# Optimization experiments

Measured on AMD Instinct MI355X. Metric: run time of the kernel, lower is better.

## Reference

```python
import jax, jax.numpy as jnp
import numpy as np
from jax.scipy.special import gammaln

# sizes (see shape_source)
N_CELLS = 1024
N_GENES = 1000
N_LATENT = 50
NB_ENC = 16          # encoder histogram bins per gene
NB_DEC = 16          # decoder mixture components (sum(n_decoder_bins))
N_HID = 16           # encoder hidden dim
N_CUTS = 4_000_000
N_FRAGS = 2_000_000
N_TOTAL_CELLS = 10_000
N_TOTAL_CUTS = 50_000_000
BN_EPS = 1e-5


def _normal_logprob(x, loc, scale):
    z = (x - loc) / scale
    return -0.5 * z * z - jnp.log(scale) - 0.5 * jnp.log(2.0 * jnp.pi)


def setup_inputs() -> dict:
    key = jax.random.key(0)
    ks = jax.random.split(key, 20)
    cut_coordinates = jax.random.uniform(ks[0], (N_CUTS,), dtype=jnp.float32)
    cut_cell = jax.random.randint(ks[1], (N_CUTS,), 0, N_CELLS)
    cut_local_gene_ix = jax.random.randint(ks[2], (N_CUTS,), 0, N_GENES)
    cut_local_cellxgene_ix = cut_cell * N_GENES + cut_local_gene_ix
    local_cellxgene_ix = jax.random.randint(ks[3], (N_FRAGS,), 0, N_CELLS * N_GENES)
    genes_oi = jnp.arange(N_GENES)
    cells_oi = jnp.arange(N_CELLS)
    eps = jax.random.normal(ks[4], (N_CELLS, N_LATENT), dtype=jnp.float32)
    n_in = N_GENES * NB_ENC
    enc_W1 = jax.random.normal(ks[5], (n_in, N_HID)) * (1.0 / np.sqrt(n_in))
    enc_b1 = jnp.zeros((N_HID,))
    bn_gamma = jnp.ones((N_HID,))
    bn_beta = jnp.zeros((N_HID,))
    W_loc = jax.random.normal(ks[6], (N_HID, N_LATENT)) * (1.0 / np.sqrt(N_HID))
    b_loc = jnp.zeros((N_LATENT,))
    W_scale = jax.random.normal(ks[7], (N_HID, N_LATENT)) * (1.0 / np.sqrt(N_HID))
    b_scale = jnp.zeros((N_LATENT,))
    logit_weight = jax.random.normal(ks[8], (N_GENES, N_LATENT, NB_DEC)) * 0.05
    rho_weight = jax.random.normal(ks[9], (N_GENES, N_LATENT)) * 0.05
    baseline_heights = jax.random.normal(ks[10], (N_GENES, NB_DEC)) * 0.1
    libsize = jax.random.randint(ks[11], (N_TOTAL_CELLS,), 1000, 20000)
    rho_bias = jax.random.uniform(ks[12], (N_GENES,), minval=1e-4, maxval=1e-2)
    return dict(
        cut_coordinates=cut_coordinates, eps=eps,
        enc_W1=enc_W1, enc_b1=enc_b1, bn_gamma=bn_gamma, bn_beta=bn_beta,
        W_loc=W_loc, b_loc=b_loc, W_scale=W_scale, b_scale=b_scale,
        logit_weight=logit_weight, rho_weight=rho_weight,
        baseline_heights=baseline_heights, rho_bias=rho_bias,
        cut_local_cellxgene_ix=cut_local_cellxgene_ix,
        cut_local_gene_ix=cut_local_gene_ix,
        local_cellxgene_ix=local_cellxgene_ix,
        genes_oi=genes_oi, cells_oi=cells_oi, libsize=libsize,
    )


def reference(cut_coordinates, eps, enc_W1, enc_b1, bn_gamma, bn_beta,
              W_loc, b_loc, W_scale, b_scale, logit_weight, rho_weight,
              baseline_heights, rho_bias, cut_local_cellxgene_ix,
              cut_local_gene_ix, local_cellxgene_ix, genes_oi, cells_oi,
              libsize):
    n_cells = cells_oi.shape[0]
    n_genes = genes_oi.shape[0]

    # ---- Encoder: digitize + bincount histogram ----
    bin_enc = jnp.minimum(jnp.floor(cut_coordinates * NB_ENC), NB_ENC - 1).astype(jnp.int32)
    digitized = bin_enc + cut_local_cellxgene_ix.astype(jnp.int32) * NB_ENC
    counts = jax.ops.segment_sum(jnp.ones_like(cut_coordinates), digitized,
                                 num_segments=n_cells * n_genes * NB_ENC)
    x = jnp.log1p(counts.reshape(n_cells, n_genes * NB_ENC))  # [C, G*NB]

    h = x @ enc_W1 + enc_b1
    mu = h.mean(axis=0)
    var = h.var(axis=0)  # biased, matches torch BN in train mode
    h = (h - mu) / jnp.sqrt(var + BN_EPS) * bn_gamma + bn_beta
    h = jax.nn.relu(h)
    loc = h @ W_loc + b_loc                 # [C, L]
    scale = jnp.exp(h @ W_scale + b_scale)  # [C, L]

    # ---- latent sample + KL ----
    q_scale = scale * 0.1
    latent = loc + q_scale * eps
    latent_kl = (_normal_logprob(latent, 0.0, 1.0)
                 - _normal_logprob(latent, loc, q_scale)) * (N_TOTAL_CELLS / n_cells)

    # ---- Decoder (n_layers=0: per-gene linear heads) ----
    lw = logit_weight[genes_oi]                       # [G, L, K]
    rw = rho_weight[genes_oi]                         # [G, L]
    mixture_delta = jnp.einsum('cl,glk->cgk', latent, lw)  # [C, G, K]
    rho_delta = jnp.einsum('cl,gl->cg', latent, rw)        # [C, G]
    md_cxg = mixture_delta.reshape(n_cells * n_genes, NB_DEC)
    md_cut = md_cxg[cut_local_cellxgene_ix]           # [N_CUTS, K] gather
    mixture_delta_kl = _normal_logprob(lw, 0.0, 0.1)

    # ---- mixture likelihood: piecewise-constant spline density per cut ----
    logits = baseline_heights[cut_local_gene_ix] + md_cut  # [N_CUTS, K]
    logp = jax.nn.log_softmax(logits, axis=-1)
    bin_dec = jnp.minimum(jnp.floor(cut_coordinates * NB_DEC), NB_DEC - 1).astype(jnp.int32)
    likelihood_mixture = (jnp.take_along_axis(logp, bin_dec[:, None], axis=1)[:, 0]
                          + jnp.log(float(NB_DEC)))

    # ---- fragment-count Poisson likelihood ----
    fragexpr = (rho_bias[genes_oi][None, :] * jnp.exp(rho_delta)
                * libsize[cells_oi].astype(jnp.float32)[:, None])  # [C, G]
    fragmentcounts = jax.ops.segment_sum(
        jnp.ones((local_cellxgene_ix.shape[0],), jnp.float32),
        local_cellxgene_ix, num_segments=n_cells * n_genes
    ).reshape(n_cells, n_genes)
    likelihood_frag = (fragmentcounts * jnp.log(fragexpr) - fragexpr
                       - gammaln(fragmentcounts + 1.0))

    rho_delta_kl = _normal_logprob(rw, 0.0, 0.1)

    likelihood = (likelihood_mixture.sum() * (N_TOTAL_CUTS / cut_coordinates.shape[0])
                  + likelihood_frag.sum() * (N_TOTAL_CELLS / n_cells))
    elbo = (-likelihood - latent_kl.sum() - mixture_delta_kl.sum()
            - rho_delta_kl.sum())
    return elbo
```

## Files before the change

### kernel.cpp

```cpp
#include <hip/hip_runtime.h>
#include <hip/hip_bf16.h>
#include <math.h>


#define G_      1000
#define C_      1024
#define L_      50
#define K_      16
#define NHID_   16
#define CUT_SCALE   12.5f
#define CELL_SCALE  9.765625f

#define CHUNK_    6144
#define RCAP_CUT  18432
#define RCAP_FRAG 9216

#define GCNTC_OFF  0ull
#define GCNTF_OFF  1024ull
#define DONE_OFF   2048ull
#define DACC_OFF   6400ull
#define HT_OFF     6912ull
#define ZERO_BYTES 72448ull
#define LATBF_OFF  72448ull
#define LWT_OFF    203520ull
#define ENTC_OFF   2251520ull
#define ENTF_OFF   11688704ull
#define MERGED_OFF 16407296ull
#define FRAGU8_OFF 24599296ull
#define LATT_OFF   25623296ull
#define WS_NEED    25828096ull

typedef __attribute__((ext_vector_type(8))) short short8;
typedef __attribute__((ext_vector_type(4))) float f32x4;

__device__ __constant__ float LGT[32] = {
    0.0f, 0.0f, 0.6931471805599453f, 1.791759469228055f, 3.1780538303479458f,
    4.787491742782046f, 6.579251212010101f, 8.525161361065415f,
    10.60460290274525f, 12.801827480081469f, 15.104412573075516f,
    17.502307845873887f, 19.987214495661885f, 22.552163853123425f,
    25.19122118273868f, 27.89927138384089f, 30.671860106080672f,
    33.50507345013689f, 36.39544520803305f, 39.339884187199495f,
    42.335616460753485f, 45.38013889847691f, 48.47118135183523f,
    51.60667556776438f, 54.78472939811232f, 58.00360522298052f,
    61.261701761002f, 64.55753862700633f, 67.88974313718154f,
    71.25703896716801f, 74.65823634883016f, 78.0922235533153f };

__device__ __forceinline__ double atomAddF64(double* p, double v) {
    return __hip_atomic_fetch_add(p, v, __ATOMIC_RELAXED,
                                  __HIP_MEMORY_SCOPE_AGENT);
}

__device__ __forceinline__ float block_sum_256(float v) {
    __shared__ float sm[256];
    int t = threadIdx.x;
    __syncthreads();
    sm[t] = v;
    __syncthreads();
#pragma unroll
    for (int s = 128; s > 0; s >>= 1) {
        if (t < s) sm[t] += sm[t + s];
        __syncthreads();
    }
    return sm[0];
}

__global__ __launch_bounds__(256)
void part_kernel(const int* __restrict__ cut_ix,
                 const float* __restrict__ coord,
                 const int* __restrict__ frag_ix,
                 unsigned int* __restrict__ gcnt_c,
                 unsigned int* __restrict__ gcnt_f,
                 unsigned short* __restrict__ entc,
                 unsigned short* __restrict__ entf,
                 const float* __restrict__ lw,
                 const float* __restrict__ rw,
                 __hip_bfloat16* __restrict__ lwT,
                 double* __restrict__ dacc,
                 int n_cuts, int n_frags, int ncc, int nblk_part) {
    int t = threadIdx.x;
    int bid = blockIdx.x;
    if (bid >= nblk_part) {
        int r = bid - nblk_part;
        if (r < 256) {
            for (int g = r; g < G_; g += 256) {
                for (int i = t; i < L_ * K_; i += 256) {
                    float v = lw[(size_t)g * (L_ * K_) + i];
                    lwT[(size_t)g * 1024 + (i & 15) * 64 + (i >> 4)] =
                        __float2bfloat16(v);
                }
                for (int i = t; i < 16 * 14; i += 256) {
                    int n = i / 14, l = 50 + (i % 14);
                    lwT[(size_t)g * 1024 + n * 64 + l] = __float2bfloat16(0.f);
                }
            }
        } else {
            const int NTOT = G_ * L_ * K_ + G_ * L_;
            int wb = r - 256;
            float s = 0.f;
            for (int i = wb * 256 + t; i < NTOT; i += 256 * 256) {
                float w = (i < G_ * L_ * K_) ? lw[i] : rw[i - G_ * L_ * K_];
                s += fmaf(-50.f * w, w, 1.3836465597893733f);
            }
            s = block_sum_256(s);
            if (t == 0) atomAddF64(&dacc[wb & 63], (double)(-s));
        }
        return;
    }
    __shared__ unsigned int cnt[256], excl[256], cur[256], gbas[256];
    __shared__ unsigned short stage[CHUNK_];
    __shared__ unsigned char bkof[CHUNK_];
    bool isCut = (bid < ncc);
    int blk = isCut ? bid : bid - ncc;
    const int* idx = isCut ? cut_ix : frag_ix;
    int n = isCut ? n_cuts : n_frags;
    int rcap = isCut ? RCAP_CUT : RCAP_FRAG;
    unsigned int* gcount = isCut ? gcnt_c : gcnt_f;
    unsigned short* ent = isCut ? entc : entf;
    int i0 = blk * CHUNK_;
    cnt[t] = 0;
    int4 I[6]; float4 X[6];
    unsigned int vm;
    bool full = (i0 + CHUNK_ <= n);
    if (full) {
        const int4* ip = (const int4*)(idx + i0);
#pragma unroll
        for (int k = 0; k < 6; ++k) I[k] = ip[k * 256 + t];
        if (isCut) {
            const float4* xp = (const float4*)(coord + i0);
#pragma unroll
            for (int k = 0; k < 6; ++k) X[k] = xp[k * 256 + t];
        }
        vm = 0xFFFFFFu;
    } else {
        vm = 0;
#pragma unroll
        for (int k = 0; k < 6; ++k) {
            int r0 = i0 + (k * 256 + t) * 4;
            int* Ii = (int*)&I[k]; float* Xi = (float*)&X[k];
#pragma unroll
            for (int u = 0; u < 4; ++u) {
                bool v = (r0 + u) < n;
                if (v) vm |= 1u << (k * 4 + u);
                Ii[u] = v ? idx[r0 + u] : 0;
                Xi[u] = (v && isCut) ? coord[r0 + u] : 0.f;
            }
        }
    }
    __syncthreads();
#pragma unroll
    for (int k = 0; k < 6; ++k) {
        const int* Ii = (const int*)&I[k];
        const float* Xi = (const float*)&X[k];
#pragma unroll
        for (int u = 0; u < 4; ++u) {
            if (vm & (1u << (k * 4 + u))) {
                int ix = Ii[u];
                int c = ix / G_;
                int g = ix - c * G_;
                unsigned int bk;
                if (isCut) {
                    int b = (int)(Xi[u] * 16.f); b = b > 15 ? 15 : b;
                    bk = ((unsigned)(c >> 6) << 4) | ((unsigned)(g * K_ + b) >> 10);
                } else {
                    bk = ((unsigned)(c >> 6) << 4) | ((unsigned)g >> 6);
                }
                atomicAdd(&cnt[bk], 1u);
            }
        }
    }
    __syncthreads();
    if (t < 64) {
        unsigned int c0 = cnt[t * 4 + 0], c1 = cnt[t * 4 + 1];
        unsigned int c2 = cnt[t * 4 + 2], c3 = cnt[t * 4 + 3];
        unsigned int tot = c0 + c1 + c2 + c3;
        unsigned int run = tot;
#pragma unroll
        for (int o = 1; o < 64; o <<= 1) {
            unsigned int v = __shfl_up(run, o, 64);
            if (t >= o) run += v;
        }
        unsigned int base = run - tot;
        excl[t * 4 + 0] = base;
        excl[t * 4 + 1] = base + c0;
        excl[t * 4 + 2] = base + c0 + c1;
        excl[t * 4 + 3] = base + c0 + c1 + c2;
    }
    __syncthreads();
    gbas[t] = cnt[t] ? atomicAdd(&gcount[t], cnt[t]) : 0u;
    cur[t] = excl[t];
    __syncthreads();
#pragma unroll
    for (int k = 0; k < 6; ++k) {
        const int* Ii = (const int*)&I[k];
        const float* Xi = (const float*)&X[k];
#pragma unroll
        for (int u = 0; u < 4; ++u) {
            if (vm & (1u << (k * 4 + u))) {
                int ix = Ii[u];
                int c = ix / G_;
                int g = ix - c * G_;
                unsigned int bk; unsigned short e;
                if (isCut) {
                    int b = (int)(Xi[u] * 16.f); b = b > 15 ? 15 : b;
                    int bin = g * K_ + b;
                    bk = ((unsigned)(c >> 6) << 4) | ((unsigned)bin >> 10);
                    e = (unsigned short)(((c & 63) << 10) | (bin & 1023));
                } else {
                    bk = ((unsigned)(c >> 6) << 4) | ((unsigned)g >> 6);
                    e = (unsigned short)(((c & 63) << 6) | (g & 63));
                }
                unsigned int p = atomicAdd(&cur[bk], 1u);
                stage[p] = e;
                bkof[p] = (unsigned char)bk;
            }
        }
    }
    __syncthreads();
    int total = n - i0; if (total > CHUNK_) total = CHUNK_;
    for (int p = t; p < total; p += 256) {
        unsigned int bk = bkof[p];
        unsigned int dst = gbas[bk] + (p - excl[bk]);
        if (dst < (unsigned)rcap)
            ent[(size_t)bk * rcap + dst] = stage[p];
    }
}

__global__ __launch_bounds__(256)
void mid_kernel(const unsigned int* __restrict__ gcnt_c,
                const unsigned short* __restrict__ entc,
                const unsigned int* __restrict__ gcnt_f,
                const unsigned short* __restrict__ entf,
                const float* __restrict__ W1,
                unsigned int* __restrict__ merged,
                unsigned int* __restrict__ fragw,
                float* __restrict__ hT) {
    __shared__ unsigned int h[8192];
    __shared__ float w1s[4096];
    int t = threadIdx.x;
    int bid = blockIdx.x;
    if (bid < 256) {
        int bk = bid;
        int cg = bk >> 4, bc = bk & 15;
        for (int i = t; i < 8192; i += 256) h[i] = 0;
        __syncthreads();
        unsigned int count = gcnt_c[bk];
        if (count > RCAP_CUT) count = RCAP_CUT;
        const unsigned int* e32 = (const unsigned int*)(entc + (size_t)bk * RCAP_CUT);
        unsigned int npair = count >> 1;
        for (unsigned int base = 0; base < npair; base += 1024) {
            unsigned int w[4]; bool val[4];
#pragma unroll
            for (int u = 0; u < 4; ++u) {
                unsigned int p = base + u * 256 + t;
                val[u] = (p < npair);
                w[u] = val[u] ? e32[p] : 0u;
            }
#pragma unroll
            for (int u = 0; u < 4; ++u) {
                if (val[u]) {
                    unsigned int v0 = w[u] & 0xffffu, v1 = w[u] >> 16;
                    unsigned int c0 = v0 >> 10, c1 = v1 >> 10;
                    atomicAdd(&h[(v0 & 1023u) * 8 + (c0 >> 3)],
                              1u << ((c0 & 7) * 4));
                    atomicAdd(&h[(v1 & 1023u) * 8 + (c1 >> 3)],
                              1u << ((c1 & 7) * 4));
                }
            }
        }
        if (t == 0 && (count & 1u)) {
            unsigned int v = ((const unsigned short*)e32)[count - 1];
            unsigned int c0 = v >> 10;
            atomicAdd(&h[(v & 1023u) * 8 + (c0 >> 3)], 1u << ((c0 & 7) * 4));
        }
        __syncthreads();
        for (int i = t; i < 8192; i += 256) {
            int bin = bc * 1024 + (i >> 3);
            if (bin < 16000)
                merged[(unsigned)bin * 128u + (unsigned)cg * 8u + (i & 7)] = h[i];
        }
        int c_lo = t & 63, sub = t >> 6;
        float acc[NHID_];
#pragma unroll
        for (int j = 0; j < NHID_; ++j) acc[j] = 0.f;
        int sh = (c_lo & 7) * 4;
        for (int qq = 0; qq < 4; ++qq) {
            __syncthreads();
            int wbase = (bc * 1024 + qq * 256) * NHID_;
#pragma unroll
            for (int r = 0; r < 16; ++r) {
                int i = r * 256 + t;
                int gi = wbase + i;
                w1s[i] = (gi < 16000 * NHID_) ? W1[gi] : 0.f;
            }
            __syncthreads();
            const float4* w1v = (const float4*)w1s;
            int rl0 = qq * 256 + sub * 64;
#pragma unroll 2
            for (int bl = 0; bl < 64; ++bl) {
                int row = bc * 1024 + rl0 + bl;
                if (row < 16000) {
                    int rh = rl0 + bl;
                    int rw2 = sub * 64 + bl;
                    unsigned int w = h[rh * 8 + (c_lo >> 3)];
                    float xv = __logf((float)(((w >> sh) & 0xfu) + 1u));
                    float4 wa = w1v[rw2 * 4 + 0];
                    float4 wb = w1v[rw2 * 4 + 1];
                    float4 wc = w1v[rw2 * 4 + 2];
                    float4 wd = w1v[rw2 * 4 + 3];
                    acc[0] = fmaf(xv, wa.x, acc[0]);  acc[1] = fmaf(xv, wa.y, acc[1]);
                    acc[2] = fmaf(xv, wa.z, acc[2]);  acc[3] = fmaf(xv, wa.w, acc[3]);
                    acc[4] = fmaf(xv, wb.x, acc[4]);  acc[5] = fmaf(xv, wb.y, acc[5]);
                    acc[6] = fmaf(xv, wb.z, acc[6]);  acc[7] = fmaf(xv, wb.w, acc[7]);
                    acc[8] = fmaf(xv, wc.x, acc[8]);  acc[9] = fmaf(xv, wc.y, acc[9]);
                    acc[10] = fmaf(xv, wc.z, acc[10]); acc[11] = fmaf(xv, wc.w, acc[11]);
                    acc[12] = fmaf(xv, wd.x, acc[12]); acc[13] = fmaf(xv, wd.y, acc[13]);
                    acc[14] = fmaf(xv, wd.z, acc[14]); acc[15] = fmaf(xv, wd.w, acc[15]);
                }
            }
        }
        __syncthreads();
        float* sp = (float*)w1s;
#pragma unroll
        for (int j = 0; j < NHID_; ++j) sp[sub * 1024 + j * 64 + c_lo] = acc[j];
        __syncthreads();
        for (int i = t; i < 1024; i += 256) {
            int j = i >> 6, c = i & 63;
            float v = sp[j * 64 + c] + sp[1024 + j * 64 + c]
                    + sp[2048 + j * 64 + c] + sp[3072 + j * 64 + c];
            atomicAdd(&hT[j * C_ + cg * 64 + c], v);
        }
    } else {
        int bk = bid - 256, cg = bk >> 4, gc = bk & 15;
        for (int i = t; i < 2048; i += 256) h[i] = 0;
        __syncthreads();
        unsigned int count = gcnt_f[bk];
        if (count > RCAP_FRAG) count = RCAP_FRAG;
        const unsigned short* e = entf + (size_t)bk * RCAP_FRAG;
#pragma unroll 4
        for (unsigned int p = t; p < count; p += 256) {
            unsigned int v = e[p];
            unsigned int g_lo = v & 63u;
            unsigned int c_lo = (v >> 6) & 63u;
            atomicAdd(&h[g_lo * 32 + (c_lo >> 1)], 1u << ((c_lo & 1) * 16));
        }
        __syncthreads();
        for (int i = t; i < 1024; i += 256) {
            int g_lo = i >> 4, wb = i & 15;
            unsigned int lo = h[g_lo * 32 + wb * 2];
            unsigned int hi = h[g_lo * 32 + wb * 2 + 1];
            unsigned int outv = (lo & 0xffu) | (((lo >> 16) & 0xffu) << 8)
                              | ((hi & 0xffu) << 16) | (((hi >> 16) & 0xffu) << 24);
            int g = gc * 64 + g_lo;
            if (g < G_)
                fragw[(unsigned)g * 256u + (unsigned)cg * 16u + wb] = outv;
        }
    }
}

__global__ __launch_bounds__(256)
void latent_kernel(const float* __restrict__ hT,
                   const float* __restrict__ gamma,
                   const float* __restrict__ beta,
                   const float* __restrict__ W_loc,
                   const float* __restrict__ b_loc,
                   const float* __restrict__ W_scale,
                   const float* __restrict__ b_scale,
                   const float* __restrict__ eps,
                   float* __restrict__ latT,
                   __hip_bfloat16* __restrict__ latbf,
                   double* __restrict__ dacc) {
    __shared__ float scs[NHID_], shs[NHID_];
    int t = threadIdx.x;
    {
        int j = t >> 4, cl = t & 15;
        double s1 = 0.0, s2 = 0.0;
#pragma unroll 8
        for (int k = 0; k < 64; ++k) {
            float v = hT[j * C_ + cl + k * 16];
            s1 += (double)v; s2 += (double)v * (double)v;
        }
#pragma unroll
        for (int m = 1; m < 16; m <<= 1) {
            s1 += __shfl_xor(s1, m);
            s2 += __shfl_xor(s2, m);
        }
        if (cl == 0) {
            double mean = s1 * (1.0 / C_);
            double var = s2 * (1.0 / C_) - mean * mean;
            float rstd = rsqrtf((float)var + 1e-5f);
            float sc = gamma[j] * rstd;
            scs[j] = sc;
            shs[j] = beta[j] - (float)mean * sc;
        }
    }
    __syncthreads();
    int idx = blockIdx.x * 256 + t;
    float kl = 0.f;
    {
        int c = idx / L_;
        int l = idx - c * L_;
        float hb[NHID_];
#pragma unroll
        for (int j = 0; j < NHID_; ++j) {
            float v = fmaf(hT[j * C_ + c], scs[j], shs[j]);
            hb[j] = v > 0.f ? v : 0.f;
        }
        float loc = b_loc[l], ls = b_scale[l];
#pragma unroll
        for (int j = 0; j < NHID_; ++j) {
            loc = fmaf(hb[j], W_loc[j * L_ + l], loc);
            ls  = fmaf(hb[j], W_scale[j * L_ + l], ls);
        }
        float qs = 0.1f * __expf(ls);
        float e = eps[idx];
        float lat = fmaf(qs, e, loc);
        latT[(size_t)l * C_ + c] = lat;
        latbf[c * 64 + l] = __float2bfloat16(lat);
        if (l < 14) latbf[c * 64 + 50 + l] = __float2bfloat16(0.f);
        float z = (lat - loc) / qs;
        kl = fmaf(-0.5f * lat, lat, fmaf(0.5f * z, z, __logf(qs)));
    }
    float s = block_sum_256(kl);
    if (threadIdx.x == 0)
        atomAddF64(&dacc[blockIdx.x & 63], (double)(-CELL_SCALE * s));
}

__global__ __launch_bounds__(256)
void mixpois_kernel(const __hip_bfloat16* __restrict__ latbf,
                    const __hip_bfloat16* __restrict__ lwT,
                    const unsigned int* __restrict__ merged,
                    const float* __restrict__ baseline,
                    const float* __restrict__ latT,
                    const float* __restrict__ rw,
                    const float* __restrict__ rho_bias,
                    const int* __restrict__ libsize,
                    const unsigned char* __restrict__ fragb,
                    double* __restrict__ dacc,
                    unsigned int* __restrict__ done,
                    float* __restrict__ out) {
    int g = blockIdx.x;
    int y = blockIdx.y;
    int t = threadIdx.x;
    int lane = t & 63;
    int wv = t >> 6;
    int s16 = lane & 15;
    int quad = lane >> 4;
    const __hip_bfloat16* bb = lwT + (size_t)g * 1024 + s16 * 64 + quad * 8;
    short8 lw1 = *(const short8*)bb;
    short8 lw2 = *(const short8*)(bb + 32);
    const float4 bl4 = *(const float4*)(baseline + g * K_ + quad * 4);
    const unsigned int* mrow =
        merged + (size_t)(g * K_ + quad * 4) * 128u;
    float partial = 0.f;
    int cwave = y * 256 + wv * 64;
#pragma unroll
    for (int mt = 0; mt < 4; ++mt) {
        int c0 = cwave + mt * 16;
        const __hip_bfloat16* aa = latbf + (size_t)(c0 + s16) * 64 + quad * 8;
        short8 la1 = *(const short8*)aa;
        short8 la2 = *(const short8*)(aa + 32);
        f32x4 d = {bl4.x, bl4.y, bl4.z, bl4.w};
        d = __builtin_amdgcn_mfma_f32_16x16x32_bf16(lw1, la1, d, 0, 0, 0);
        d = __builtin_amdgcn_mfma_f32_16x16x32_bf16(lw2, la2, d, 0, 0, 0);
        float m = fmaxf(fmaxf(d[0], d[1]), fmaxf(d[2], d[3]));
        m = fmaxf(m, __shfl_xor(m, 16));
        m = fmaxf(m, __shfl_xor(m, 32));
        float e0 = __expf(d[0] - m), e1 = __expf(d[1] - m);
        float e2 = __expf(d[2] - m), e3 = __expf(d[3] - m);
        float S = (e0 + e1) + (e2 + e3);
        S += __shfl_xor(S, 16);
        S += __shfl_xor(S, 32);
        float lse = m + __logf(S);
        int cp = c0 + s16;
        unsigned int widx = (unsigned)cp >> 3;
        int sb = (cp & 7) * 4;
#pragma unroll
        for (int r = 0; r < 4; ++r) {
            float cnt = (float)((mrow[r * 128u + widx] >> sb) & 0xfu);
            partial = fmaf(cnt, d[r] - lse, partial);
        }
    }
    float v;
    {
        int c = y * 256 + t;
        const float* rwg = rw + (size_t)g * L_;
        float rho = 0.f;
#pragma unroll 10
        for (int l = 0; l < L_; ++l)
            rho = fmaf(latT[l * C_ + c], rwg[l], rho);
        unsigned int fc = fragb[(size_t)g * C_ + c];
        float fe = rho_bias[g] * __expf(rho) * (float)libsize[c];
        float lf = fmaf((float)fc, __logf(fe), -fe) - LGT[fc > 31u ? 31u : fc];
        v = fmaf(-CUT_SCALE, partial, -CELL_SCALE * lf);
    }
    float contrib = block_sum_256(v);
    __shared__ int lastflag;
    if (threadIdx.x == 0) {
        lastflag = 0;
        int slot = blockIdx.x & 63;
        double oldv = atomAddF64(&dacc[slot], (double)contrib);
        unsigned inc = 1u;
        float dep = (float)oldv;
        asm volatile("" : "+v"(inc) : "v"(dep));
        unsigned quota = ((slot < 40) ? 16u : 15u) * 4u;
        if (atomicAdd(&done[slot * 16], inc) == quota - 1u) {
            if (atomicAdd(&done[1024], 1u) == 63u) lastflag = 1;
        }
    }
    __syncthreads();
    if (lastflag) {
        if (t < 64) {
            double dv = atomAddF64(&dacc[t], 0.0);
#pragma unroll
            for (int m = 1; m < 64; m <<= 1) dv += __shfl_xor(dv, m);
            if (t == 0)
                out[0] = (float)(dv - 138629436.11198905);
        }
    }
}

extern "C" void kernel_launch(void* const* d_in, const int* in_sizes, int n_in,
                              void* d_out, int out_size, void* d_ws, size_t ws_size,
                              hipStream_t stream) {
    const float* cut_coord = (const float*)d_in[0];
    const float* eps       = (const float*)d_in[1];
    const float* enc_W1    = (const float*)d_in[2];
    const float* bn_gamma  = (const float*)d_in[4];
    const float* bn_beta   = (const float*)d_in[5];
    const float* W_loc     = (const float*)d_in[6];
    const float* b_loc     = (const float*)d_in[7];
    const float* W_scale   = (const float*)d_in[8];
    const float* b_scale   = (const float*)d_in[9];
    const float* logit_w   = (const float*)d_in[10];
    const float* rho_w     = (const float*)d_in[11];
    const float* baseline  = (const float*)d_in[12];
    const float* rho_bias  = (const float*)d_in[13];
    const int* cut_cxg     = (const int*)d_in[14];
    const int* frag_ix     = (const int*)d_in[16];
    const int* libsize     = (const int*)d_in[19];

    int n_cuts  = in_sizes[0];
    int n_frags = in_sizes[16];

    char* ws = (char*)d_ws;
    unsigned int*   gcnt_c = (unsigned int*)(ws + GCNTC_OFF);
    unsigned int*   gcnt_f = (unsigned int*)(ws + GCNTF_OFF);
    unsigned int*   done   = (unsigned int*)(ws + DONE_OFF);
    double*         dacc   = (double*)(ws + DACC_OFF);
    float*          hT     = (float*)(ws + HT_OFF);
    __hip_bfloat16* latbf  = (__hip_bfloat16*)(ws + LATBF_OFF);
    __hip_bfloat16* lwT    = (__hip_bfloat16*)(ws + LWT_OFF);
    unsigned short* entc   = (unsigned short*)(ws + ENTC_OFF);
    unsigned short* entf   = (unsigned short*)(ws + ENTF_OFF);
    unsigned int*   merged = (unsigned int*)(ws + MERGED_OFF);
    unsigned int*   fragw  = (unsigned int*)(ws + FRAGU8_OFF);
    float*          latT   = (float*)(ws + LATT_OFF);
    float*          out    = (float*)d_out;

    int ncc = (n_cuts + CHUNK_ - 1) / CHUNK_;
    int ncf = (n_frags + CHUNK_ - 1) / CHUNK_;
    int nblk_part = ncc + ncf;

    hipMemsetAsync(ws, 0, ZERO_BYTES, stream);

    part_kernel<<<nblk_part + 512, 256, 0, stream>>>(
        cut_cxg, cut_coord, frag_ix, gcnt_c, gcnt_f, entc, entf,
        logit_w, rho_w, lwT, dacc,
        n_cuts, n_frags, ncc, nblk_part);
    mid_kernel<<<512, 256, 0, stream>>>(
        gcnt_c, entc, gcnt_f, entf, enc_W1, merged, fragw, hT);
    latent_kernel<<<(C_ * L_) / 256, 256, 0, stream>>>(
        hT, bn_gamma, bn_beta, W_loc, b_loc, W_scale, b_scale,
        eps, latT, latbf, dacc);
    mixpois_kernel<<<dim3(G_, 4), 256, 0, stream>>>(
        latbf, lwT, merged, baseline, latT, rho_w, rho_bias, libsize,
        (const unsigned char*)fragw, dacc, done, out);
}
```

Baseline: 244.5 us.

## Split each cut-histogram block into two cell halves to double parallelism

Each cut bucket in mid_kernel is now handled by two blocks, each owning 32 of the 64 cells in its cell group. The per-block packed histogram and the encoder W1 dot product are halved, which cuts shared memory per block and doubles the number of cut blocks. The goal is more parallelism and occupancy in the histogram and encoder stage. The cost is that each block still streams the whole entry list and discards entries for the other half, so entry reads double; the inner-loop row bound check is also dropped and relies on zero padding.

After: 225.3 us. 1.09x faster.

```diff
diff --git a/kernel.cpp b/kernel.cpp
--- a/kernel.cpp
+++ b/kernel.cpp
@@ -234,18 +234,19 @@
                 unsigned int* __restrict__ merged,
                 unsigned int* __restrict__ fragw,
                 float* __restrict__ hT) {
-    __shared__ unsigned int h[8192];
+    __shared__ unsigned int h[4096];
     __shared__ float w1s[4096];
     int t = threadIdx.x;
     int bid = blockIdx.x;
-    if (bid < 256) {
-        int bk = bid;
+    if (bid < 512) {
+        int bk = bid >> 1, half = bid & 1;
         int cg = bk >> 4, bc = bk & 15;
-        for (int i = t; i < 8192; i += 256) h[i] = 0;
+        for (int i = t; i < 4096; i += 256) h[i] = 0;
         __syncthreads();
         unsigned int count = gcnt_c[bk];
         if (count > RCAP_CUT) count = RCAP_CUT;
         const unsigned int* e32 = (const unsigned int*)(entc + (size_t)bk * RCAP_CUT);
+        unsigned int hsel = (unsigned)half << 5;
         unsigned int npair = count >> 1;
         for (unsigned int base = 0; base < npair; base += 1024) {
             unsigned int w[4]; bool val[4];
@@ -260,32 +261,43 @@
                 if (val[u]) {
                     unsigned int v0 = w[u] & 0xffffu, v1 = w[u] >> 16;
                     unsigned int c0 = v0 >> 10, c1 = v1 >> 10;
-                    atomicAdd(&h[(v0 & 1023u) * 8 + (c0 >> 3)],
-                              1u << ((c0 & 7) * 4));
-                    atomicAdd(&h[(v1 & 1023u) * 8 + (c1 >> 3)],
-                              1u << ((c1 & 7) * 4));
+                    if ((c0 & 32u) == hsel) {
+                        unsigned int cc = c0 & 31u;
+                        atomicAdd(&h[(v0 & 1023u) * 4 + (cc >> 3)],
+                                  1u << ((cc & 7) * 4));
+                    }
+                    if ((c1 & 32u) == hsel) {
+                        unsigned int cc = c1 & 31u;
+                        atomicAdd(&h[(v1 & 1023u) * 4 + (cc >> 3)],
+                                  1u << ((cc & 7) * 4));
+                    }
                 }
             }
         }
         if (t == 0 && (count & 1u)) {
             unsigned int v = ((const unsigned short*)e32)[count - 1];
             unsigned int c0 = v >> 10;
-            atomicAdd(&h[(v & 1023u) * 8 + (c0 >> 3)], 1u << ((c0 & 7) * 4));
-        }
-        __syncthreads();
-        for (int i = t; i < 8192; i += 256) {
-            int bin = bc * 1024 + (i >> 3);
+            if ((c0 & 32u) == hsel) {
+                unsigned int cc = c0 & 31u;
+                atomicAdd(&h[(v & 1023u) * 4 + (cc >> 3)], 1u << ((cc & 7) * 4));
+            }
+        }
+        __syncthreads();
+        for (int i = t; i < 4096; i += 256) {
+            int binlo = i >> 2, wq = i & 3;
+            int bin = bc * 1024 + binlo;
             if (bin < 16000)
-                merged[(unsigned)bin * 128u + (unsigned)cg * 8u + (i & 7)] = h[i];
-        }
-        int c_lo = t & 63, sub = t >> 6;
+                merged[(unsigned)bin * 128u + (unsigned)(cg * 8 + half * 4 + wq)]
+                    = h[i];
+        }
+        int c32 = t & 31, sub = t >> 5;
+        int sh = (c32 & 7) * 4, widx = c32 >> 3;
         float acc[NHID_];
 #pragma unroll
         for (int j = 0; j < NHID_; ++j) acc[j] = 0.f;
-        int sh = (c_lo & 7) * 4;
-        for (int qq = 0; qq < 4; ++qq) {
+        for (int q = 0; q < 4; ++q) {
             __syncthreads();
-            int wbase = (bc * 1024 + qq * 256) * NHID_;
+            int wbase = (bc * 1024 + q * 256) * NHID_;
 #pragma unroll
             for (int r = 0; r < 16; ++r) {
                 int i = r * 256 + t;
@@ -294,43 +306,41 @@
             }
             __syncthreads();
             const float4* w1v = (const float4*)w1s;
-            int rl0 = qq * 256 + sub * 64;
-#pragma unroll 2
-            for (int bl = 0; bl < 64; ++bl) {
-                int row = bc * 1024 + rl0 + bl;
-                if (row < 16000) {
-                    int rh = rl0 + bl;
-                    int rw2 = sub * 64 + bl;
-                    unsigned int w = h[rh * 8 + (c_lo >> 3)];
-                    float xv = __logf((float)(((w >> sh) & 0xfu) + 1u));
-                    float4 wa = w1v[rw2 * 4 + 0];
-                    float4 wb = w1v[rw2 * 4 + 1];
-                    float4 wc = w1v[rw2 * 4 + 2];
-                    float4 wd = w1v[rw2 * 4 + 3];
-                    acc[0] = fmaf(xv, wa.x, acc[0]);  acc[1] = fmaf(xv, wa.y, acc[1]);
-                    acc[2] = fmaf(xv, wa.z, acc[2]);  acc[3] = fmaf(xv, wa.w, acc[3]);
-                    acc[4] = fmaf(xv, wb.x, acc[4]);  acc[5] = fmaf(xv, wb.y, acc[5]);
-                    acc[6] = fmaf(xv, wb.z, acc[6]);  acc[7] = fmaf(xv, wb.w, acc[7]);
-                    acc[8] = fmaf(xv, wc.x, acc[8]);  acc[9] = fmaf(xv, wc.y, acc[9]);
-                    acc[10] = fmaf(xv, wc.z, acc[10]); acc[11] = fmaf(xv, wc.w, acc[11]);
-                    acc[12] = fmaf(xv, wd.x, acc[12]); acc[13] = fmaf(xv, wd.y, acc[13]);
-                    acc[14] = fmaf(xv, wd.z, acc[14]); acc[15] = fmaf(xv, wd.w, acc[15]);
-                }
+            int rl0 = q * 256 + sub * 32;
+#pragma unroll 4
+            for (int bl = 0; bl < 32; ++bl) {
+                int rl = rl0 + bl;
+                int rwc = sub * 32 + bl;
+                unsigned int w = h[rl * 4 + widx];
+                float xv = __logf((float)(((w >> sh) & 0xfu) + 1u));
+                float4 wa = w1v[rwc * 4 + 0];
+                float4 wb = w1v[rwc * 4 + 1];
+                float4 wc = w1v[rwc * 4 + 2];
+                float4 wd = w1v[rwc * 4 + 3];
+                acc[0] = fmaf(xv, wa.x, acc[0]);  acc[1] = fmaf(xv, wa.y, acc[1]);
+                acc[2] = fmaf(xv, wa.z, acc[2]);  acc[3] = fmaf(xv, wa.w, acc[3]);
+                acc[4] = fmaf(xv, wb.x, acc[4]);  acc[5] = fmaf(xv, wb.y, acc[5]);
+                acc[6] = fmaf(xv, wb.z, acc[6]);  acc[7] = fmaf(xv, wb.w, acc[7]);
+                acc[8] = fmaf(xv, wc.x, acc[8]);  acc[9] = fmaf(xv, wc.y, acc[9]);
+                acc[10] = fmaf(xv, wc.z, acc[10]); acc[11] = fmaf(xv, wc.w, acc[11]);
+                acc[12] = fmaf(xv, wd.x, acc[12]); acc[13] = fmaf(xv, wd.y, acc[13]);
+                acc[14] = fmaf(xv, wd.z, acc[14]); acc[15] = fmaf(xv, wd.w, acc[15]);
             }
         }
         __syncthreads();
         float* sp = (float*)w1s;
 #pragma unroll
-        for (int j = 0; j < NHID_; ++j) sp[sub * 1024 + j * 64 + c_lo] = acc[j];
-        __syncthreads();
-        for (int i = t; i < 1024; i += 256) {
-            int j = i >> 6, c = i & 63;
-            float v = sp[j * 64 + c] + sp[1024 + j * 64 + c]
-                    + sp[2048 + j * 64 + c] + sp[3072 + j * 64 + c];
-            atomicAdd(&hT[j * C_ + cg * 64 + c], v);
+        for (int j = 0; j < NHID_; ++j) sp[sub * 512 + j * 32 + c32] = acc[j];
+        __syncthreads();
+        for (int i = t; i < 512; i += 256) {
+            int j = i >> 5, cc = i & 31;
+            float v = 0.f;
+#pragma unroll
+            for (int s = 0; s < 8; ++s) v += sp[s * 512 + j * 32 + cc];
+            atomicAdd(&hT[j * C_ + cg * 64 + half * 32 + cc], v);
         }
     } else {
-        int bk = bid - 256, cg = bk >> 4, gc = bk & 15;
+        int bk = bid - 512, cg = bk >> 4, gc = bk & 15;
         for (int i = t; i < 2048; i += 256) h[i] = 0;
         __syncthreads();
         unsigned int count = gcnt_f[bk];
@@ -567,7 +577,7 @@
         cut_cxg, cut_coord, frag_ix, gcnt_c, gcnt_f, entc, entf,
         logit_w, rho_w, lwT, dacc,
         n_cuts, n_frags, ncc, nblk_part);
-    mid_kernel<<<512, 256, 0, stream>>>(
+    mid_kernel<<<768, 256, 0, stream>>>(
         gcnt_c, entc, gcnt_f, entf, enc_W1, merged, fragw, hT);
     latent_kernel<<<(C_ * L_) / 256, 256, 0, stream>>>(
         hT, bn_gamma, bn_beta, W_loc, b_loc, W_scale, b_scale,
```
